# Kernel optimization log

Hardware: AMD Instinct MI355X
Metric: run time of the kernel (lower is better)

The kernel has to match this reference:

```python
import jax, jax.numpy as jnp
import numpy as np

N = 10000       # nodes
E = 320000      # edges (avg degree 32)
F_IN = 128      # node_in_fts
F_OUT = 128     # node_out_fts
H = 4           # num_heads_node
E_IN = 64       # edge_in_fts
HOPS = 3        # nr_of_hops
SLOPE = 0.2     # LeakyReLU negative slope (GAT default)


def setup_inputs() -> dict:
    key = jax.random.key(0)
    ks = jax.random.split(key, 10)
    s = 0.05
    return {
        "node_fts": jax.random.normal(ks[0], (N, F_IN), dtype=jnp.float32),
        "edge_fts": jax.random.normal(ks[1], (E, E_IN), dtype=jnp.float32),
        "edges": jax.random.randint(ks[2], (2, E), 0, N),
        # per-hop GATConv params (all hops share dims, stacked on axis 0)
        "Ws": jax.random.normal(ks[3], (HOPS, F_IN, H * F_OUT), dtype=jnp.float32) * s,
        "Wes": jax.random.normal(ks[4], (HOPS, E_IN, H * F_OUT), dtype=jnp.float32) * s,
        "a_src": jax.random.normal(ks[5], (HOPS, H, F_OUT), dtype=jnp.float32) * s,
        "a_dst": jax.random.normal(ks[6], (HOPS, H, F_OUT), dtype=jnp.float32) * s,
        "a_edge": jax.random.normal(ks[7], (HOPS, H, F_OUT), dtype=jnp.float32) * s,
        # gated residual params
        "W_prior": jax.random.normal(ks[8], (F_OUT, F_OUT), dtype=jnp.float32) * s,
        "W_curr": jax.random.normal(ks[9], (F_OUT, F_OUT), dtype=jnp.float32) * s,
    }


def _gat_conv(x, edge_fts, src, dst, W, We, asrc, adst, aedge):
    # dense projections: [N,H,F_OUT] and [E,H,F_OUT]
    h = (x @ W).reshape(-1, H, F_OUT)
    he = (edge_fts @ We).reshape(-1, H, F_OUT)
    h_src = h[src]                                   # [E,H,F_OUT] gather
    # per-edge attention logits [E,H]
    alpha = (h_src * asrc).sum(-1) + (h[dst] * adst).sum(-1) + (he * aedge).sum(-1)
    alpha = jax.nn.leaky_relu(alpha, SLOPE)
    # segment softmax over incoming edges of each destination node
    amax = jnp.full((N, H), -jnp.inf, dtype=alpha.dtype).at[dst].max(alpha)
    w = jnp.exp(alpha - amax[dst])                   # [E,H]
    denom = jax.ops.segment_sum(w, dst, num_segments=N) + 1e-16  # [N,H]
    msg = w[:, :, None] * h_src                      # [E,H,F_OUT]
    out = jax.ops.segment_sum(msg, dst, num_segments=N) / denom[:, :, None]
    return out.mean(axis=1)                          # mean head aggregation -> [N,F_OUT]


def reference(node_fts, edge_fts, edges, Ws, Wes, a_src, a_dst, a_edge, W_prior, W_curr):
    src, dst = edges[0], edges[1]
    x = node_fts
    prior = None
    for i in range(HOPS):
        curr = _gat_conv(x, edge_fts, src, dst, Ws[i], Wes[i], a_src[i], a_dst[i], a_edge[i])
        if prior is None:
            x = curr
        else:
            gate = jax.nn.sigmoid(prior @ W_prior + curr @ W_curr)
            x = gate * curr + (1.0 - gate) * prior
        prior = x
    return x
```

## Files before the change

kernel.cpp:

```cpp
#include <hip/hip_runtime.h>
#include <hip/hip_fp16.h>

#define N_NODES 10000
#define E_EDGES 320000
#define NH 4
#define HOPS 3
#define MAXD 512

typedef _Float16 f16x8 __attribute__((ext_vector_type(8)));
typedef _Float16 f16x4 __attribute__((ext_vector_type(4)));
typedef float    f32x4 __attribute__((ext_vector_type(4)));

__global__ void k_count(const int* __restrict__ dst, int* __restrict__ counts){
  int e = blockIdx.x*256 + threadIdx.x;
  if(e < E_EDGES) atomicAdd(&counts[dst[e]], 1);
}

__global__ __launch_bounds__(1024) void k_scan(const int* __restrict__ counts,
                                               int* __restrict__ row_ptr, int* __restrict__ fillp){
  __shared__ int sm[1024];
  int t = threadIdx.x;
  const int CH = 10;
  int base = t*CH;
  int loc[CH]; int sum = 0;
  #pragma unroll
  for(int i=0;i<CH;i++){
    int v = (base+i < N_NODES) ? counts[base+i] : 0;
    loc[i] = sum; sum += v;
  }
  sm[t] = sum; __syncthreads();
  for(int off=1; off<1024; off<<=1){
    int add = (t>=off) ? sm[t-off] : 0;
    __syncthreads();
    sm[t] += add;
    __syncthreads();
  }
  int excl = (t>0) ? sm[t-1] : 0;
  #pragma unroll
  for(int i=0;i<CH;i++){
    int n = base+i;
    if(n < N_NODES){
      int e = excl + loc[i];
      row_ptr[n] = e;
      fillp[n]   = e;
    }
  }
  if(t==1023) row_ptr[N_NODES] = sm[1023];
}

__global__ void k_fill(const int* __restrict__ src, const int* __restrict__ dst,
                       int* __restrict__ fillp, int* __restrict__ csr_eid, int* __restrict__ sorted_src){
  int e = blockIdx.x*256 + threadIdx.x;
  if(e < E_EDGES){
    int d = dst[e];
    int pos = atomicAdd(&fillp[d], 1);
    csr_eid[pos] = e;
    sorted_src[pos] = src[e];
  }
}

__global__ void k_bedge(const float* __restrict__ Wes, const float* __restrict__ a_edge,
                        float* __restrict__ b_edge){
  int idx = blockIdx.x*256 + threadIdx.x;
  if(idx >= HOPS*64*NH) return;
  int hop = idx/(64*NH); int c = (idx/NH)%64; int h = idx%NH;
  const float* we = Wes + (size_t)hop*64*512 + (size_t)c*512 + h*128;
  const float* ae = a_edge + (size_t)hop*NH*128 + h*128;
  float s = 0.f;
  for(int f=0; f<128; f++) s += we[f] * ae[f];
  b_edge[idx] = s;
}

__global__ __launch_bounds__(256) void k_alpha_e(const float* __restrict__ edge_fts,
                        const int* __restrict__ csr_eid, const float* __restrict__ b_edge,
                        float* __restrict__ ae_sorted){
  __shared__ float bl[HOPS*64*NH];
  for(int i=threadIdx.x; i<HOPS*64*NH; i+=256) bl[i] = b_edge[i];
  __syncthreads();
  int pos = blockIdx.x*256 + threadIdx.x;
  if(pos >= E_EDGES) return;
  int e = csr_eid[pos];
  const float* ef = edge_fts + (size_t)e*64;
  float acc[HOPS*NH];
  #pragma unroll
  for(int i=0;i<HOPS*NH;i++) acc[i]=0.f;
  for(int c=0; c<64; c+=4){
    float4 xv = *(const float4*)(ef + c);
    float x[4] = {xv.x, xv.y, xv.z, xv.w};
    #pragma unroll
    for(int j=0;j<4;j++){
      float xc = x[j]; int cc = c+j;
      #pragma unroll
      for(int hh=0; hh<HOPS*NH; hh++){
        int hop = hh>>2, h = hh&3;
        acc[hh] += xc * bl[hop*256 + cc*4 + h];
      }
    }
  }
  #pragma unroll
  for(int hop=0; hop<HOPS; hop++){
    *(float4*)(ae_sorted + ((size_t)hop*E_EDGES + pos)*4) =
      make_float4(acc[hop*4+0], acc[hop*4+1], acc[hop*4+2], acc[hop*4+3]);
  }
}

__global__ void k_xh0(const float* __restrict__ in, _Float16* __restrict__ out){
  int i = blockIdx.x*256 + threadIdx.x;
  float4 v = *(const float4*)(in + (size_t)i*4);
  f16x4 h = { (_Float16)v.x, (_Float16)v.y, (_Float16)v.z, (_Float16)v.w };
  *(f16x4*)(out + (size_t)i*4) = h;
}

__global__ __launch_bounds__(256) void k_wt(const float* __restrict__ Ws, _Float16* __restrict__ WsT){
  __shared__ float lds[32][65];
  int b = blockIdx.x;
  int hop = b>>5, rem = b&31, kt = rem>>3, ct = rem&7;
  int k0 = kt*32, c0 = ct*64;
  int t = threadIdx.x;
  const float* wsrc = Ws + (size_t)hop*65536;
  #pragma unroll
  for(int i=0;i<8;i++){
    int u = t + i*256;
    int kk = u>>6, cc = u&63;
    lds[kk][cc] = wsrc[(size_t)(k0+kk)*512 + c0 + cc];
  }
  __syncthreads();
  _Float16* wdst = WsT + (size_t)hop*512*128;
  #pragma unroll
  for(int i=0;i<2;i++){
    int u = t + i*256;
    int c = u>>3, kq = (u&7)*4;
    f16x4 h = { (_Float16)lds[kq][c], (_Float16)lds[kq+1][c],
                (_Float16)lds[kq+2][c], (_Float16)lds[kq+3][c] };
    *(f16x4*)(wdst + (size_t)(c0+c)*128 + k0 + kq) = h;
  }
}

__global__ __launch_bounds__(256) void k_projm(const _Float16* __restrict__ xh,
                       const _Float16* __restrict__ Wt, __half* __restrict__ h_all){
  int w = threadIdx.x>>6, l = threadIdx.x&63;
  int row0 = blockIdx.x*64 + w*16;
  int col0 = blockIdx.y*64;
  int ar = l&15, ac = (l>>4)*8;
  f32x4 acc0 = {0.f,0.f,0.f,0.f}, acc1 = acc0, acc2 = acc0, acc3 = acc0;
  #pragma unroll
  for(int kk=0; kk<4; kk++){
    f16x8 a = *(const f16x8*)(xh + (size_t)(row0+ar)*128 + kk*32 + ac);
    f16x8 b0 = *(const f16x8*)(Wt + (size_t)(col0 +  0 + ar)*128 + kk*32 + ac);
    f16x8 b1 = *(const f16x8*)(Wt + (size_t)(col0 + 16 + ar)*128 + kk*32 + ac);
    f16x8 b2 = *(const f16x8*)(Wt + (size_t)(col0 + 32 + ar)*128 + kk*32 + ac);
    f16x8 b3 = *(const f16x8*)(Wt + (size_t)(col0 + 48 + ar)*128 + kk*32 + ac);
    acc0 = __builtin_amdgcn_mfma_f32_16x16x32_f16(a, b0, acc0, 0, 0, 0);
    acc1 = __builtin_amdgcn_mfma_f32_16x16x32_f16(a, b1, acc1, 0, 0, 0);
    acc2 = __builtin_amdgcn_mfma_f32_16x16x32_f16(a, b2, acc2, 0, 0, 0);
    acc3 = __builtin_amdgcn_mfma_f32_16x16x32_f16(a, b3, acc3, 0, 0, 0);
  }
  int crow = (l>>4)*4, ccol = l&15;
  #pragma unroll
  for(int r=0; r<4; r++){
    int row = row0 + crow + r;
    if(row < N_NODES){
      size_t base = (size_t)row*512 + col0 + ccol;
      h_all[base +  0] = __float2half(acc0[r]);
      h_all[base + 16] = __float2half(acc1[r]);
      h_all[base + 32] = __float2half(acc2[r]);
      h_all[base + 48] = __float2half(acc3[r]);
    }
  }
}

__global__ __launch_bounds__(256) void k_s(const __half* __restrict__ h_all, const float* __restrict__ asrc,
                    const float* __restrict__ adst, float* __restrict__ s_src, float* __restrict__ s_dst){
  int n = blockIdx.x; int t = threadIdx.x;
  int h = t>>6; int f0 = (t&63)<<1;
  __half2 hv2 = *(const __half2*)(h_all + (size_t)n*512 + (h<<7) + f0);
  float2 hv = __half22float2(hv2);
  int ai = (h<<7) + f0;
  float ps = hv.x*asrc[ai] + hv.y*asrc[ai+1];
  float pd = hv.x*adst[ai] + hv.y*adst[ai+1];
  #pragma unroll
  for(int off=32; off; off>>=1){ ps += __shfl_xor(ps,off); pd += __shfl_xor(pd,off); }
  if((t&63)==0){ s_src[n*4+h] = ps; s_dst[n*4+h] = pd; }
}

__global__ __launch_bounds__(256) void k_softagg(
    const float* __restrict__ ae, const float* __restrict__ s_src,
    const float* __restrict__ s_dst, const int* __restrict__ sorted_src,
    const int* __restrict__ row_ptr, const __half* __restrict__ h_all,
    float* __restrict__ ew_fb, float* __restrict__ xout, _Float16* __restrict__ xh)
{
  __shared__ float ws[MAXD*4];
  __shared__ int   ssm[MAXD];
  __shared__ float red[512];
  __shared__ float mred[4][4];
  __shared__ float sred[4][4];

  int n = blockIdx.x, t = threadIdx.x;
  int start = row_ptr[n], end = row_ptr[n+1];
  int deg = end - start;
  bool fits = (deg <= MAXD);
  int wv = t>>6, lane = t&63;

  float4 sd = *(const float4*)(s_dst + (size_t)n*4);
  float m0=-1e30f, m1=-1e30f, m2=-1e30f, m3=-1e30f;
  float aR[2][4];

  if(fits){
    #pragma unroll
    for(int k=0;k<2;k++){
      int pos = start + t + k*256;
      if(pos < end){
        int s = sorted_src[pos];
        float4 ss = *(const float4*)(s_src + (size_t)s*4);
        float4 av = *(const float4*)(ae + (size_t)pos*4);
        float a0 = ss.x+sd.x+av.x; a0=(a0>0.f)?a0:0.2f*a0;
        float a1 = ss.y+sd.y+av.y; a1=(a1>0.f)?a1:0.2f*a1;
        float a2 = ss.z+sd.z+av.z; a2=(a2>0.f)?a2:0.2f*a2;
        float a3 = ss.w+sd.w+av.w; a3=(a3>0.f)?a3:0.2f*a3;
        aR[k][0]=a0; aR[k][1]=a1; aR[k][2]=a2; aR[k][3]=a3;
        ssm[t + k*256] = s;
        m0=fmaxf(m0,a0); m1=fmaxf(m1,a1); m2=fmaxf(m2,a2); m3=fmaxf(m3,a3);
      }
    }
  } else {
    for(int pos=start+t; pos<end; pos+=256){
      int s = sorted_src[pos];
      float4 ss = *(const float4*)(s_src + (size_t)s*4);
      float4 av = *(const float4*)(ae + (size_t)pos*4);
      float a0 = ss.x+sd.x+av.x; a0=(a0>0.f)?a0:0.2f*a0;
      float a1 = ss.y+sd.y+av.y; a1=(a1>0.f)?a1:0.2f*a1;
      float a2 = ss.z+sd.z+av.z; a2=(a2>0.f)?a2:0.2f*a2;
      float a3 = ss.w+sd.w+av.w; a3=(a3>0.f)?a3:0.2f*a3;
      *(float4*)(ew_fb + (size_t)pos*4) = make_float4(a0,a1,a2,a3);
      m0=fmaxf(m0,a0); m1=fmaxf(m1,a1); m2=fmaxf(m2,a2); m3=fmaxf(m3,a3);
    }
  }
  #pragma unroll
  for(int off=32; off; off>>=1){
    m0=fmaxf(m0,__shfl_xor(m0,off)); m1=fmaxf(m1,__shfl_xor(m1,off));
    m2=fmaxf(m2,__shfl_xor(m2,off)); m3=fmaxf(m3,__shfl_xor(m3,off));
  }
  if(lane==0){ mred[wv][0]=m0; mred[wv][1]=m1; mred[wv][2]=m2; mred[wv][3]=m3; }
  __syncthreads();
  m0 = fmaxf(fmaxf(mred[0][0],mred[1][0]),fmaxf(mred[2][0],mred[3][0]));
  m1 = fmaxf(fmaxf(mred[0][1],mred[1][1]),fmaxf(mred[2][1],mred[3][1]));
  m2 = fmaxf(fmaxf(mred[0][2],mred[1][2]),fmaxf(mred[2][2],mred[3][2]));
  m3 = fmaxf(fmaxf(mred[0][3],mred[1][3]),fmaxf(mred[2][3],mred[3][3]));

  float s0=0.f,s1=0.f,s2=0.f,s3=0.f;
  if(fits){
    #pragma unroll
    for(int k=0;k<2;k++){
      int pos = start + t + k*256;
      if(pos < end){
        float w0=__expf(aR[k][0]-m0), w1=__expf(aR[k][1]-m1);
        float w2=__expf(aR[k][2]-m2), w3=__expf(aR[k][3]-m3);
        int sl = (t + k*256)*4;
        ws[sl]=w0; ws[sl+1]=w1; ws[sl+2]=w2; ws[sl+3]=w3;
        s0+=w0; s1+=w1; s2+=w2; s3+=w3;
      }
    }
  } else {
    for(int pos=start+t; pos<end; pos+=256){
      float4 a = *(const float4*)(ew_fb + (size_t)pos*4);
      float w0=__expf(a.x-m0), w1=__expf(a.y-m1), w2=__expf(a.z-m2), w3=__expf(a.w-m3);
      *(float4*)(ew_fb + (size_t)pos*4) = make_float4(w0,w1,w2,w3);
      s0+=w0; s1+=w1; s2+=w2; s3+=w3;
    }
  }
  #pragma unroll
  for(int off=32; off; off>>=1){
    s0+=__shfl_xor(s0,off); s1+=__shfl_xor(s1,off);
    s2+=__shfl_xor(s2,off); s3+=__shfl_xor(s3,off);
  }
  if(lane==0){ sred[wv][0]=s0; sred[wv][1]=s1; sred[wv][2]=s2; sred[wv][3]=s3; }
  __syncthreads();

  int slot = t>>6;
  int l = t&63;
  int h = l>>4;
  int f8 = (l&15)*8;
  float dh = sred[0][h]+sred[1][h]+sred[2][h]+sred[3][h];
  float inv = 1.f/(dh + 1e-16f);
  float acc[8] = {0.f,0.f,0.f,0.f,0.f,0.f,0.f,0.f};
  for(int p = start + slot; p < end; p += 4){
    int sl = p - start;
    int s; float w;
    if(fits){ s = ssm[sl]; w = ws[sl*4 + h]; }
    else    { s = sorted_src[p]; w = ew_fb[(size_t)p*4 + h]; }
    const __half* hp = h_all + (size_t)s*512 + (h<<7) + f8;
    float4 raw = *(const float4*)hp;
    const __half2* hh = (const __half2*)&raw;
    float2 c0 = __half22float2(hh[0]);
    float2 c1 = __half22float2(hh[1]);
    float2 c2 = __half22float2(hh[2]);
    float2 c3 = __half22float2(hh[3]);
    acc[0]+=w*c0.x; acc[1]+=w*c0.y; acc[2]+=w*c1.x; acc[3]+=w*c1.y;
    acc[4]+=w*c2.x; acc[5]+=w*c2.y; acc[6]+=w*c3.x; acc[7]+=w*c3.y;
  }
  #pragma unroll
  for(int i=0;i<8;i++) acc[i]*=inv;
  int flat = (h<<7) + f8;
  if(slot==0){
    #pragma unroll
    for(int i=0;i<8;i++) red[flat+i] = acc[i];
  }
  __syncthreads();
  #pragma unroll
  for(int sg=1; sg<4; sg++){
    if(slot==sg){
      #pragma unroll
      for(int i=0;i<8;i++) red[flat+i] += acc[i];
    }
    __syncthreads();
  }
  if(t < 128){
    float v = 0.25f*(red[t] + red[128+t] + red[256+t] + red[384+t]);
    xout[(size_t)n*128 + t] = v;
    if(xh) xh[(size_t)n*128 + t] = (_Float16)v;
  }
}

__global__ __launch_bounds__(256) void k_gate2(const float* __restrict__ prior, const float* __restrict__ curr,
                       const float* __restrict__ Wp, const float* __restrict__ Wc,
                       float* __restrict__ xnew, _Float16* __restrict__ xh){
  __shared__ float pr[32][132];
  __shared__ float cu[32][132];
  int t = threadIdx.x;
  int n0 = blockIdx.x*32;
  int c0 = blockIdx.y*64;
  #pragma unroll
  for(int i=0;i<4;i++){
    int u = t + i*256;
    int row = u>>5, c4 = (u&31)<<2;
    float4 v = make_float4(0.f,0.f,0.f,0.f), w = v;
    if(n0+row < N_NODES){
      v = *(const float4*)(prior + (size_t)(n0+row)*128 + c4);
      w = *(const float4*)(curr  + (size_t)(n0+row)*128 + c4);
    }
    *(float4*)&pr[row][c4] = v;
    *(float4*)&cu[row][c4] = w;
  }
  __syncthreads();
  int tc = t&15, tr = t>>4;
  int r0 = tr*2, cc = c0 + tc*4;
  float accp[2][4] = {{0.f,0.f,0.f,0.f},{0.f,0.f,0.f,0.f}};
  float accc[2][4] = {{0.f,0.f,0.f,0.f},{0.f,0.f,0.f,0.f}};
  #pragma unroll 4
  for(int k=0;k<128;k++){
    float4 wp = *(const float4*)(Wp + (size_t)k*128 + cc);
    float4 wc = *(const float4*)(Wc + (size_t)k*128 + cc);
    #pragma unroll
    for(int i=0;i<2;i++){
      float ap = pr[r0+i][k], ac = cu[r0+i][k];
      accp[i][0]+=ap*wp.x; accp[i][1]+=ap*wp.y; accp[i][2]+=ap*wp.z; accp[i][3]+=ap*wp.w;
      accc[i][0]+=ac*wc.x; accc[i][1]+=ac*wc.y; accc[i][2]+=ac*wc.z; accc[i][3]+=ac*wc.w;
    }
  }
  #pragma unroll
  for(int i=0;i<2;i++){
    int row = n0 + r0 + i;
    if(row < N_NODES){
      float oj[4];
      #pragma unroll
      for(int j=0;j<4;j++){
        float z = accp[i][j]+accc[i][j];
        float g = 1.f/(1.f+__expf(-z));
        oj[j] = g*cu[r0+i][cc - c0 + c0 + j] + (1.f-g)*pr[r0+i][cc + j];
      }
      *(float4*)(xnew + (size_t)row*128 + cc) = make_float4(oj[0],oj[1],oj[2],oj[3]);
      if(xh){
        f16x4 hv = { (_Float16)oj[0], (_Float16)oj[1], (_Float16)oj[2], (_Float16)oj[3] };
        *(f16x4*)(xh + (size_t)row*128 + cc) = hv;
      }
    }
  }
}

extern "C" void kernel_launch(void* const* d_in, const int* in_sizes, int n_in,
                              void* d_out, int out_size, void* d_ws, size_t ws_size,
                              hipStream_t stream){
  (void)in_sizes; (void)n_in; (void)out_size; (void)ws_size;
  const float* node_fts = (const float*)d_in[0];
  const float* edge_fts = (const float*)d_in[1];
  const int*   edges    = (const int*)d_in[2];
  const float* Ws       = (const float*)d_in[3];
  const float* Wes      = (const float*)d_in[4];
  const float* a_src    = (const float*)d_in[5];
  const float* a_dst    = (const float*)d_in[6];
  const float* a_edge   = (const float*)d_in[7];
  const float* W_prior  = (const float*)d_in[8];
  const float* W_curr   = (const float*)d_in[9];

  char* ws = (char*)d_ws;
  size_t off = 0;
  auto alloc = [&](size_t bytes)->void*{
    void* p = ws + off;
    off += (bytes + 255) & ~(size_t)255;
    return p;
  };
  int*       counts     = (int*)      alloc((size_t)N_NODES*4);
  int*       row_ptr    = (int*)      alloc((size_t)(N_NODES+1)*4);
  int*       fillp      = (int*)      alloc((size_t)N_NODES*4);
  int*       csr_eid    = (int*)      alloc((size_t)E_EDGES*4);
  int*       sorted_src = (int*)      alloc((size_t)E_EDGES*4);
  float*     b_edge     = (float*)    alloc((size_t)HOPS*64*NH*4);
  float*     ae_sorted  = (float*)    alloc((size_t)HOPS*E_EDGES*NH*4);
  __half*    h_all      = (__half*)   alloc((size_t)N_NODES*512*2);
  float*     s_src      = (float*)    alloc((size_t)N_NODES*NH*4);
  float*     s_dst      = (float*)    alloc((size_t)N_NODES*NH*4);
  float*     ew_fb      = (float*)    alloc((size_t)E_EDGES*NH*4);
  float*     xbuf       = (float*)    alloc((size_t)N_NODES*128*4);
  float*     curbuf     = (float*)    alloc((size_t)N_NODES*128*4);
  _Float16*  xh         = (_Float16*) alloc((size_t)10112*128*2);
  _Float16*  WsT        = (_Float16*) alloc((size_t)HOPS*512*128*2);

  const int* src = edges;
  const int* dst = edges + E_EDGES;

  (void)hipMemsetAsync(counts, 0, (size_t)N_NODES*4, stream);
  k_count<<<(E_EDGES+255)/256, 256, 0, stream>>>(dst, counts);
  k_scan<<<1, 1024, 0, stream>>>(counts, row_ptr, fillp);
  k_fill<<<(E_EDGES+255)/256, 256, 0, stream>>>(src, dst, fillp, csr_eid, sorted_src);
  k_bedge<<<3, 256, 0, stream>>>(Wes, a_edge, b_edge);
  k_alpha_e<<<(E_EDGES+255)/256, 256, 0, stream>>>(edge_fts, csr_eid, b_edge, ae_sorted);
  k_wt<<<96, 256, 0, stream>>>(Ws, WsT);
  k_xh0<<<1250, 256, 0, stream>>>(node_fts, xh);

  for(int hop=0; hop<HOPS; hop++){
    k_projm<<<dim3(157, 8), 256, 0, stream>>>(xh, WsT + (size_t)hop*512*128, h_all);
    k_s<<<N_NODES, 256, 0, stream>>>(h_all, a_src + (size_t)hop*512, a_dst + (size_t)hop*512, s_src, s_dst);
    float* xout = (hop==0) ? xbuf : curbuf;
    k_softagg<<<N_NODES, 256, 0, stream>>>(ae_sorted + (size_t)hop*E_EDGES*4, s_src, s_dst,
                                           sorted_src, row_ptr, h_all, ew_fb, xout,
                                           (hop==0) ? xh : (_Float16*)nullptr);
    if(hop > 0){
      float* xnew = (hop == HOPS-1) ? (float*)d_out : xbuf;
      k_gate2<<<dim3(313, 2), 256, 0, stream>>>(xbuf, curbuf, W_prior, W_curr, xnew,
                                                (hop < HOPS-1) ? xh : (_Float16*)nullptr);
    }
  }
}
```

Measured before the change: 360.4 us.

## Fuse setup kernels, coalesce edge and projection stores, shrink softagg reductions

Merges the fp16 casts of node features and weights and the edge-bias precompute into one setup kernel. k_alpha_e now reads edge features in original order and scatters through a stored per-edge position, and k_projm stages its output tile in LDS so it can write 16-byte coalesced stores. k_s handles four nodes per block with vector loads. In k_softagg the in-register path drops to degree 256 and the serialized four-step LDS reduction becomes one sync plus a sum. Nodes with degree above 256 now take the slower fallback path.

```diff
diff --git a/kernel.cpp b/kernel.cpp
--- a/kernel.cpp
+++ b/kernel.cpp
@@ -5,7 +5,7 @@
 #define E_EDGES 320000
 #define NH 4
 #define HOPS 3
-#define MAXD 512
+#define MAXD 256
 
 typedef _Float16 f16x8 __attribute__((ext_vector_type(8)));
 typedef _Float16 f16x4 __attribute__((ext_vector_type(4)));
@@ -49,37 +49,70 @@
 }
 
 __global__ void k_fill(const int* __restrict__ src, const int* __restrict__ dst,
-                       int* __restrict__ fillp, int* __restrict__ csr_eid, int* __restrict__ sorted_src){
+                       int* __restrict__ fillp, int* __restrict__ pos_e, int* __restrict__ sorted_src){
   int e = blockIdx.x*256 + threadIdx.x;
   if(e < E_EDGES){
     int d = dst[e];
     int pos = atomicAdd(&fillp[d], 1);
-    csr_eid[pos] = e;
+    pos_e[e] = pos;
     sorted_src[pos] = src[e];
   }
 }
 
-__global__ void k_bedge(const float* __restrict__ Wes, const float* __restrict__ a_edge,
-                        float* __restrict__ b_edge){
-  int idx = blockIdx.x*256 + threadIdx.x;
-  if(idx >= HOPS*64*NH) return;
-  int hop = idx/(64*NH); int c = (idx/NH)%64; int h = idx%NH;
-  const float* we = Wes + (size_t)hop*64*512 + (size_t)c*512 + h*128;
-  const float* ae = a_edge + (size_t)hop*NH*128 + h*128;
-  float s = 0.f;
-  for(int f=0; f<128; f++) s += we[f] * ae[f];
-  b_edge[idx] = s;
+__global__ __launch_bounds__(256) void k_setup(const float* __restrict__ node_fts, _Float16* __restrict__ xh,
+                       const float* __restrict__ Ws, _Float16* __restrict__ WsT,
+                       const float* __restrict__ Wes, const float* __restrict__ a_edge,
+                       float* __restrict__ b_edge){
+  __shared__ float lds[32][65];
+  int b = blockIdx.x, t = threadIdx.x;
+  if(b < 1250){
+    int i = b*256 + t;
+    float4 v = *(const float4*)(node_fts + (size_t)i*4);
+    f16x4 h = { (_Float16)v.x, (_Float16)v.y, (_Float16)v.z, (_Float16)v.w };
+    *(f16x4*)(xh + (size_t)i*4) = h;
+  } else if(b < 1346){
+    int b2 = b - 1250;
+    int hop = b2>>5, rem = b2&31, kt = rem>>3, ct = rem&7;
+    int k0 = kt*32, c0 = ct*64;
+    const float* wsrc = Ws + (size_t)hop*65536;
+    #pragma unroll
+    for(int i=0;i<8;i++){
+      int u = t + i*256;
+      int kk = u>>6, cc = u&63;
+      lds[kk][cc] = wsrc[(size_t)(k0+kk)*512 + c0 + cc];
+    }
+    __syncthreads();
+    _Float16* wdst = WsT + (size_t)hop*512*128;
+    #pragma unroll
+    for(int i=0;i<2;i++){
+      int u = t + i*256;
+      int c = u>>3, kq = (u&7)*4;
+      f16x4 h = { (_Float16)lds[kq][c], (_Float16)lds[kq+1][c],
+                  (_Float16)lds[kq+2][c], (_Float16)lds[kq+3][c] };
+      *(f16x4*)(wdst + (size_t)(c0+c)*128 + k0 + kq) = h;
+    }
+  } else {
+    int idx = (b-1346)*256 + t;
+    if(idx < HOPS*64*NH){
+      int hop = idx/(64*NH); int c = (idx/NH)%64; int h = idx%NH;
+      const float* we = Wes + (size_t)hop*64*512 + (size_t)c*512 + h*128;
+      const float* ae = a_edge + (size_t)hop*NH*128 + h*128;
+      float s = 0.f;
+      for(int f=0; f<128; f++) s += we[f] * ae[f];
+      b_edge[idx] = s;
+    }
+  }
 }
 
 __global__ __launch_bounds__(256) void k_alpha_e(const float* __restrict__ edge_fts,
-                        const int* __restrict__ csr_eid, const float* __restrict__ b_edge,
+                        const int* __restrict__ pos_e, const float* __restrict__ b_edge,
                         float* __restrict__ ae_sorted){
   __shared__ float bl[HOPS*64*NH];
   for(int i=threadIdx.x; i<HOPS*64*NH; i+=256) bl[i] = b_edge[i];
   __syncthreads();
-  int pos = blockIdx.x*256 + threadIdx.x;
-  if(pos >= E_EDGES) return;
-  int e = csr_eid[pos];
+  int e = blockIdx.x*256 + threadIdx.x;
+  if(e >= E_EDGES) return;
+  int pos = pos_e[e];
   const float* ef = edge_fts + (size_t)e*64;
   float acc[HOPS*NH];
   #pragma unroll
@@ -104,48 +137,18 @@
   }
 }
 
-__global__ void k_xh0(const float* __restrict__ in, _Float16* __restrict__ out){
-  int i = blockIdx.x*256 + threadIdx.x;
-  float4 v = *(const float4*)(in + (size_t)i*4);
-  f16x4 h = { (_Float16)v.x, (_Float16)v.y, (_Float16)v.z, (_Float16)v.w };
-  *(f16x4*)(out + (size_t)i*4) = h;
-}
-
-__global__ __launch_bounds__(256) void k_wt(const float* __restrict__ Ws, _Float16* __restrict__ WsT){
-  __shared__ float lds[32][65];
-  int b = blockIdx.x;
-  int hop = b>>5, rem = b&31, kt = rem>>3, ct = rem&7;
-  int k0 = kt*32, c0 = ct*64;
-  int t = threadIdx.x;
-  const float* wsrc = Ws + (size_t)hop*65536;
-  #pragma unroll
-  for(int i=0;i<8;i++){
-    int u = t + i*256;
-    int kk = u>>6, cc = u&63;
-    lds[kk][cc] = wsrc[(size_t)(k0+kk)*512 + c0 + cc];
-  }
-  __syncthreads();
-  _Float16* wdst = WsT + (size_t)hop*512*128;
-  #pragma unroll
-  for(int i=0;i<2;i++){
-    int u = t + i*256;
-    int c = u>>3, kq = (u&7)*4;
-    f16x4 h = { (_Float16)lds[kq][c], (_Float16)lds[kq+1][c],
-                (_Float16)lds[kq+2][c], (_Float16)lds[kq+3][c] };
-    *(f16x4*)(wdst + (size_t)(c0+c)*128 + k0 + kq) = h;
-  }
-}
-
 __global__ __launch_bounds__(256) void k_projm(const _Float16* __restrict__ xh,
                        const _Float16* __restrict__ Wt, __half* __restrict__ h_all){
+  __shared__ __align__(16) __half tile[64][72];
   int w = threadIdx.x>>6, l = threadIdx.x&63;
-  int row0 = blockIdx.x*64 + w*16;
+  int rowb = blockIdx.x*64;
+  int row0 = rowb + w*16;
   int col0 = blockIdx.y*64;
   int ar = l&15, ac = (l>>4)*8;
   f32x4 acc0 = {0.f,0.f,0.f,0.f}, acc1 = acc0, acc2 = acc0, acc3 = acc0;
   #pragma unroll
   for(int kk=0; kk<4; kk++){
-    f16x8 a = *(const f16x8*)(xh + (size_t)(row0+ar)*128 + kk*32 + ac);
+    f16x8 a  = *(const f16x8*)(xh + (size_t)(row0+ar)*128 + kk*32 + ac);
     f16x8 b0 = *(const f16x8*)(Wt + (size_t)(col0 +  0 + ar)*128 + kk*32 + ac);
     f16x8 b1 = *(const f16x8*)(Wt + (size_t)(col0 + 16 + ar)*128 + kk*32 + ac);
     f16x8 b2 = *(const f16x8*)(Wt + (size_t)(col0 + 32 + ar)*128 + kk*32 + ac);
@@ -158,29 +161,47 @@
   int crow = (l>>4)*4, ccol = l&15;
   #pragma unroll
   for(int r=0; r<4; r++){
-    int row = row0 + crow + r;
-    if(row < N_NODES){
-      size_t base = (size_t)row*512 + col0 + ccol;
-      h_all[base +  0] = __float2half(acc0[r]);
-      h_all[base + 16] = __float2half(acc1[r]);
-      h_all[base + 32] = __float2half(acc2[r]);
-      h_all[base + 48] = __float2half(acc3[r]);
-    }
+    int tr = w*16 + crow + r;
+    tile[tr][ccol     ] = __float2half(acc0[r]);
+    tile[tr][ccol + 16] = __float2half(acc1[r]);
+    tile[tr][ccol + 32] = __float2half(acc2[r]);
+    tile[tr][ccol + 48] = __float2half(acc3[r]);
+  }
+  __syncthreads();
+  #pragma unroll
+  for(int i=0;i<2;i++){
+    int u = threadIdx.x + i*256;
+    int row = u>>3, cq = (u&7)*8;
+    int grow = rowb + row;
+    if(grow < N_NODES)
+      *(float4*)(h_all + (size_t)grow*512 + col0 + cq) = *(const float4*)&tile[row][cq];
   }
 }
 
 __global__ __launch_bounds__(256) void k_s(const __half* __restrict__ h_all, const float* __restrict__ asrc,
                     const float* __restrict__ adst, float* __restrict__ s_src, float* __restrict__ s_dst){
-  int n = blockIdx.x; int t = threadIdx.x;
-  int h = t>>6; int f0 = (t&63)<<1;
-  __half2 hv2 = *(const __half2*)(h_all + (size_t)n*512 + (h<<7) + f0);
-  float2 hv = __half22float2(hv2);
-  int ai = (h<<7) + f0;
-  float ps = hv.x*asrc[ai] + hv.y*asrc[ai+1];
-  float pd = hv.x*adst[ai] + hv.y*adst[ai+1];
-  #pragma unroll
-  for(int off=32; off; off>>=1){ ps += __shfl_xor(ps,off); pd += __shfl_xor(pd,off); }
-  if((t&63)==0){ s_src[n*4+h] = ps; s_dst[n*4+h] = pd; }
+  int nw = blockIdx.x*4 + (threadIdx.x>>6);
+  int l = threadIdx.x&63;
+  if(nw >= N_NODES) return;
+  int h = l>>4, f8 = (l&15)*8;
+  const __half* hp = h_all + (size_t)nw*512 + (h<<7) + f8;
+  float4 raw = *(const float4*)hp;
+  const __half2* hh = (const __half2*)&raw;
+  float2 c0 = __half22float2(hh[0]);
+  float2 c1 = __half22float2(hh[1]);
+  float2 c2 = __half22float2(hh[2]);
+  float2 c3 = __half22float2(hh[3]);
+  float4 a0 = *(const float4*)(asrc + (h<<7) + f8);
+  float4 a1 = *(const float4*)(asrc + (h<<7) + f8 + 4);
+  float4 d0 = *(const float4*)(adst + (h<<7) + f8);
+  float4 d1 = *(const float4*)(adst + (h<<7) + f8 + 4);
+  float ps = c0.x*a0.x + c0.y*a0.y + c1.x*a0.z + c1.y*a0.w
+           + c2.x*a1.x + c2.y*a1.y + c3.x*a1.z + c3.y*a1.w;
+  float pd = c0.x*d0.x + c0.y*d0.y + c1.x*d0.z + c1.y*d0.w
+           + c2.x*d1.x + c2.y*d1.y + c3.x*d1.z + c3.y*d1.w;
+  #pragma unroll
+  for(int off=1; off<16; off<<=1){ ps += __shfl_xor(ps,off); pd += __shfl_xor(pd,off); }
+  if((l&15)==0){ s_src[nw*4+h] = ps; s_dst[nw*4+h] = pd; }
 }
 
 __global__ __launch_bounds__(256) void k_softagg(
@@ -191,7 +212,7 @@
 {
   __shared__ float ws[MAXD*4];
   __shared__ int   ssm[MAXD];
-  __shared__ float red[512];
+  __shared__ float red2[4][520];
   __shared__ float mred[4][4];
   __shared__ float sred[4][4];
 
@@ -203,24 +224,21 @@
 
   float4 sd = *(const float4*)(s_dst + (size_t)n*4);
   float m0=-1e30f, m1=-1e30f, m2=-1e30f, m3=-1e30f;
-  float aR[2][4];
+  float aR[4];
 
   if(fits){
-    #pragma unroll
-    for(int k=0;k<2;k++){
-      int pos = start + t + k*256;
-      if(pos < end){
-        int s = sorted_src[pos];
-        float4 ss = *(const float4*)(s_src + (size_t)s*4);
-        float4 av = *(const float4*)(ae + (size_t)pos*4);
-        float a0 = ss.x+sd.x+av.x; a0=(a0>0.f)?a0:0.2f*a0;
-        float a1 = ss.y+sd.y+av.y; a1=(a1>0.f)?a1:0.2f*a1;
-        float a2 = ss.z+sd.z+av.z; a2=(a2>0.f)?a2:0.2f*a2;
-        float a3 = ss.w+sd.w+av.w; a3=(a3>0.f)?a3:0.2f*a3;
-        aR[k][0]=a0; aR[k][1]=a1; aR[k][2]=a2; aR[k][3]=a3;
-        ssm[t + k*256] = s;
-        m0=fmaxf(m0,a0); m1=fmaxf(m1,a1); m2=fmaxf(m2,a2); m3=fmaxf(m3,a3);
-      }
+    if(t < deg){
+      int pos = start + t;
+      int s = sorted_src[pos];
+      float4 ss = *(const float4*)(s_src + (size_t)s*4);
+      float4 av = *(const float4*)(ae + (size_t)pos*4);
+      float a0 = ss.x+sd.x+av.x; a0=(a0>0.f)?a0:0.2f*a0;
+      float a1 = ss.y+sd.y+av.y; a1=(a1>0.f)?a1:0.2f*a1;
+      float a2 = ss.z+sd.z+av.z; a2=(a2>0.f)?a2:0.2f*a2;
+      float a3 = ss.w+sd.w+av.w; a3=(a3>0.f)?a3:0.2f*a3;
+      aR[0]=a0; aR[1]=a1; aR[2]=a2; aR[3]=a3;
+      ssm[t] = s;
+      m0=a0; m1=a1; m2=a2; m3=a3;
     }
   } else {
     for(int pos=start+t; pos<end; pos+=256){
@@ -249,16 +267,12 @@
 
   float s0=0.f,s1=0.f,s2=0.f,s3=0.f;
   if(fits){
-    #pragma unroll
-    for(int k=0;k<2;k++){
-      int pos = start + t + k*256;
-      if(pos < end){
-        float w0=__expf(aR[k][0]-m0), w1=__expf(aR[k][1]-m1);
-        float w2=__expf(aR[k][2]-m2), w3=__expf(aR[k][3]-m3);
-        int sl = (t + k*256)*4;
-        ws[sl]=w0; ws[sl+1]=w1; ws[sl+2]=w2; ws[sl+3]=w3;
-        s0+=w0; s1+=w1; s2+=w2; s3+=w3;
-      }
+    if(t < deg){
+      float w0=__expf(aR[0]-m0), w1=__expf(aR[1]-m1);
+      float w2=__expf(aR[2]-m2), w3=__expf(aR[3]-m3);
+      int sl = t*4;
+      ws[sl]=w0; ws[sl+1]=w1; ws[sl+2]=w2; ws[sl+3]=w3;
+      s0=w0; s1=w1; s2=w2; s3=w3;
     }
   } else {
     for(int pos=start+t; pos<end; pos+=256){
@@ -298,24 +312,16 @@
     acc[0]+=w*c0.x; acc[1]+=w*c0.y; acc[2]+=w*c1.x; acc[3]+=w*c1.y;
     acc[4]+=w*c2.x; acc[5]+=w*c2.y; acc[6]+=w*c3.x; acc[7]+=w*c3.y;
   }
-  #pragma unroll
-  for(int i=0;i<8;i++) acc[i]*=inv;
   int flat = (h<<7) + f8;
-  if(slot==0){
+  #pragma unroll
+  for(int i=0;i<8;i++) red2[slot][flat+i] = acc[i]*inv;
+  __syncthreads();
+  if(t < 128){
+    float v = 0.f;
     #pragma unroll
-    for(int i=0;i<8;i++) red[flat+i] = acc[i];
-  }
-  __syncthreads();
-  #pragma unroll
-  for(int sg=1; sg<4; sg++){
-    if(slot==sg){
-      #pragma unroll
-      for(int i=0;i<8;i++) red[flat+i] += acc[i];
-    }
-    __syncthreads();
-  }
-  if(t < 128){
-    float v = 0.25f*(red[t] + red[128+t] + red[256+t] + red[384+t]);
+    for(int s=0;s<4;s++)
+      v += red2[s][t] + red2[s][128+t] + red2[s][256+t] + red2[s][384+t];
+    v *= 0.25f;
     xout[(size_t)n*128 + t] = v;
     if(xh) xh[(size_t)n*128 + t] = (_Float16)v;
   }
@@ -366,7 +372,7 @@
       for(int j=0;j<4;j++){
         float z = accp[i][j]+accc[i][j];
         float g = 1.f/(1.f+__expf(-z));
-        oj[j] = g*cu[r0+i][cc - c0 + c0 + j] + (1.f-g)*pr[r0+i][cc + j];
+        oj[j] = g*cu[r0+i][cc + j] + (1.f-g)*pr[r0+i][cc + j];
       }
       *(float4*)(xnew + (size_t)row*128 + cc) = make_float4(oj[0],oj[1],oj[2],oj[3]);
       if(xh){
@@ -402,7 +408,7 @@
   int*       counts     = (int*)      alloc((size_t)N_NODES*4);
   int*       row_ptr    = (int*)      alloc((size_t)(N_NODES+1)*4);
   int*       fillp      = (int*)      alloc((size_t)N_NODES*4);
-  int*       csr_eid    = (int*)      alloc((size_t)E_EDGES*4);
+  int*       pos_e      = (int*)      alloc((size_t)E_EDGES*4);
   int*       sorted_src = (int*)      alloc((size_t)E_EDGES*4);
   float*     b_edge     = (float*)    alloc((size_t)HOPS*64*NH*4);
   float*     ae_sorted  = (float*)    alloc((size_t)HOPS*E_EDGES*NH*4);
@@ -421,15 +427,13 @@
   (void)hipMemsetAsync(counts, 0, (size_t)N_NODES*4, stream);
   k_count<<<(E_EDGES+255)/256, 256, 0, stream>>>(dst, counts);
   k_scan<<<1, 1024, 0, stream>>>(counts, row_ptr, fillp);
-  k_fill<<<(E_EDGES+255)/256, 256, 0, stream>>>(src, dst, fillp, csr_eid, sorted_src);
-  k_bedge<<<3, 256, 0, stream>>>(Wes, a_edge, b_edge);
-  k_alpha_e<<<(E_EDGES+255)/256, 256, 0, stream>>>(edge_fts, csr_eid, b_edge, ae_sorted);
-  k_wt<<<96, 256, 0, stream>>>(Ws, WsT);
-  k_xh0<<<1250, 256, 0, stream>>>(node_fts, xh);
+  k_fill<<<(E_EDGES+255)/256, 256, 0, stream>>>(src, dst, fillp, pos_e, sorted_src);
+  k_setup<<<1349, 256, 0, stream>>>(node_fts, xh, Ws, WsT, Wes, a_edge, b_edge);
+  k_alpha_e<<<(E_EDGES+255)/256, 256, 0, stream>>>(edge_fts, pos_e, b_edge, ae_sorted);
 
   for(int hop=0; hop<HOPS; hop++){
     k_projm<<<dim3(157, 8), 256, 0, stream>>>(xh, WsT + (size_t)hop*512*128, h_all);
-    k_s<<<N_NODES, 256, 0, stream>>>(h_all, a_src + (size_t)hop*512, a_dst + (size_t)hop*512, s_src, s_dst);
+    k_s<<<2500, 256, 0, stream>>>(h_all, a_src + (size_t)hop*512, a_dst + (size_t)hop*512, s_src, s_dst);
     float* xout = (hop==0) ? xbuf : curbuf;
     k_softagg<<<N_NODES, 256, 0, stream>>>(ae_sorted + (size_t)hop*E_EDGES*4, s_src, s_dst,
                                            sorted_src, row_ptr, h_all, ew_fb, xout,
```

Result: faster. 346.1 us (-4.0%).
